# Performance work log

Measured on AMD Instinct MI355X. Metric: run time of the kernel, lower is better.

The kernel has to match this reference:

```python
import jax, jax.numpy as jnp
import numpy as np

DT = 1.0            # neuron_config.base_config.dt (ms)
TAU_MEM = 10.0      # membrane time constant (ms)
SURROGATE_BETA = 1.0  # surrogate sigmoid sharpness for spike nonlinearity

B, P = 256, 4096


def setup_inputs() -> dict:
    key = jax.random.key(0)
    k1, k2, k3, k4 = jax.random.split(key, 4)
    return {
        "external_input": jax.random.normal(k1, (B, P), dtype=jnp.float32),
        "lateral_weights": jax.random.normal(k2, (P, P), dtype=jnp.float32) * 0.1,
        "population_activity": jax.random.uniform(k3, (P,), dtype=jnp.float32),
        "v": jax.random.normal(k4, (B, P), dtype=jnp.float32),
        "threshold": jnp.ones((B, P), dtype=jnp.float32),
    }


def reference(external_input, lateral_weights, population_activity, v, threshold):
    P_ = external_input.shape[1]
    # lateral inhibition: zero self-connections (inhibition_mask = eye == 0)
    masked_w = lateral_weights * (1.0 - jnp.eye(P_, dtype=lateral_weights.dtype))
    lateral = population_activity @ masked_w              # [P]
    total_input = external_input - lateral[None, :]        # [B, P]
    # vectorized adaptive-threshold LIF step across the whole population
    decay = jnp.exp(jnp.asarray(-DT / TAU_MEM, dtype=v.dtype))
    v_new = decay * v + total_input                        # [B, P]
    u = (v_new - threshold) / SURROGATE_BETA
    soft = jax.nn.sigmoid(u)
    hard = (v_new > threshold).astype(v.dtype)
    # straight-through spike: hard forward, sigmoid-surrogate gradient
    spikes = jax.lax.stop_gradient(hard - soft) + soft     # [B, P]
    return spikes
```

## Files before the change

kernel.cpp:

```cpp
#include <hip/hip_runtime.h>


#define PP 4096
#define BB 256

using f4 = __attribute__((ext_vector_type(4))) float;

constexpr int ROWS_PER_CHUNK = 32;
constexpr int NCHUNK = PP / ROWS_PER_CHUNK;
constexpr int COLS_PER_TILE = 512;
constexpr int NTILE = PP / COLS_PER_TILE;

__global__ __launch_bounds__(256)
void lateral_partial(const float* __restrict__ w, const float* __restrict__ pa,
                     double* __restrict__ part) {
    const int tile = blockIdx.x & (NTILE - 1);
    const int rch  = blockIdx.x >> 3;
    const int c    = tile * COLS_PER_TILE + (int)threadIdx.x * 2;
    const int r0   = rch * ROWS_PER_CHUNK;
    double a0 = 0.0, a1 = 0.0;
#pragma unroll
    for (int k = 0; k < ROWS_PER_CHUNK; ++k) {
        const int i = r0 + k;
        const double p = (double)pa[i];
        const float2 wv = *reinterpret_cast<const float2*>(w + (size_t)i * PP + c);
        a0 += p * (double)wv.x;
        a1 += p * (double)wv.y;
    }
    *reinterpret_cast<double2*>(part + (size_t)rch * PP + c) = make_double2(a0, a1);
}

__global__ __launch_bounds__(256)
void lateral_reduce(const double* __restrict__ part, const float* __restrict__ w,
                    const float* __restrict__ pa, double* __restrict__ lat) {
    __shared__ double sh[256];
    const int t   = (int)threadIdx.x;
    const int cj  = t & 31;
    const int grp = t >> 5;
    const int col = blockIdx.x * 32 + cj;
    double s = 0.0;
#pragma unroll
    for (int k = 0; k < NCHUNK / 8; ++k)
        s += part[(size_t)(grp * (NCHUNK / 8) + k) * PP + col];
    sh[t] = s;
    __syncthreads();
    if (t < 128) sh[t] += sh[t + 128];
    __syncthreads();
    if (t < 64)  sh[t] += sh[t + 64];
    __syncthreads();
    if (t < 32) {
        double r = sh[t] + sh[t + 32];
        lat[col] = r - (double)pa[col] * (double)w[(size_t)col * (PP + 1)];
    }
}

__global__ __launch_bounds__(256)
void spike(const float* __restrict__ ext, const float* __restrict__ v,
           const float* __restrict__ thr, const double* __restrict__ lat,
           float* __restrict__ out) {
    const size_t t = ((size_t)blockIdx.x * 256 + threadIdx.x) * 4;
    const int j = (int)(t & (PP - 1));
    const f4 e  = *reinterpret_cast<const f4*>(ext + t);
    const f4 vv = *reinterpret_cast<const f4*>(v + t);
    const f4 th = *reinterpret_cast<const f4*>(thr + t);
    const double2 lA = *reinterpret_cast<const double2*>(lat + j);
    const double2 lB = *reinterpret_cast<const double2*>(lat + j + 2);
    const double dec = 0.90483741803595952;
    f4 o;
    o.x = (dec * (double)vv.x + (double)e.x - lA.x > (double)th.x) ? 1.0f : 0.0f;
    o.y = (dec * (double)vv.y + (double)e.y - lA.y > (double)th.y) ? 1.0f : 0.0f;
    o.z = (dec * (double)vv.z + (double)e.z - lB.x > (double)th.z) ? 1.0f : 0.0f;
    o.w = (dec * (double)vv.w + (double)e.w - lB.y > (double)th.w) ? 1.0f : 0.0f;
    *reinterpret_cast<f4*>(out + t) = o;
}

extern "C" void kernel_launch(void* const* d_in, const int* in_sizes, int n_in,
                              void* d_out, int out_size, void* d_ws, size_t ws_size,
                              hipStream_t stream) {
    const float* ext = (const float*)d_in[0];
    const float* w   = (const float*)d_in[1];
    const float* pa  = (const float*)d_in[2];
    const float* v   = (const float*)d_in[3];
    const float* thr = (const float*)d_in[4];
    float* out = (float*)d_out;

    double* part = (double*)d_ws;
    double* lat  = part + (size_t)NCHUNK * PP;

    lateral_partial<<<NTILE * NCHUNK, 256, 0, stream>>>(w, pa, part);
    lateral_reduce<<<PP / 32, 256, 0, stream>>>(part, w, pa, lat);
    spike<<<(BB * PP) / (4 * 256), 256, 0, stream>>>(ext, v, thr, lat, out);
}
```

Measured before the change: 112.3 us.

## Fuse lateral reduction into spike kernel and stage partials in output buffer

Merges the column reduction and the spike evaluation into one kernel, so each block reduces 16 columns and then writes the spikes for all 256 batch rows of those columns. This drops one launch and the global round trip through the lateral vector. The partial sums now live in the output buffer rather than the workspace. Their layout is interleaved so that each block only overwrites its own partials, and only after it has read them. The partial kernel also now loads four columns per thread. The trade-off is that the spike phase makes narrow 64-byte row accesses that coalesce less well than the earlier fully contiguous pass.

After: 111.9 us. About the same (-0.3%).

```diff
diff --git a/kernel.cpp b/kernel.cpp
--- a/kernel.cpp
+++ b/kernel.cpp
@@ -8,70 +8,84 @@
 
 constexpr int ROWS_PER_CHUNK = 32;
 constexpr int NCHUNK = PP / ROWS_PER_CHUNK;
-constexpr int COLS_PER_TILE = 512;
+constexpr int COLS_PER_TILE = 1024;
 constexpr int NTILE = PP / COLS_PER_TILE;
+constexpr int STRIPE = 16;
+constexpr int NSTRIPE = PP / STRIPE;
 
 __global__ __launch_bounds__(256)
 void lateral_partial(const float* __restrict__ w, const float* __restrict__ pa,
-                     double* __restrict__ part) {
+                     double* __restrict__ pd) {
     const int tile = blockIdx.x & (NTILE - 1);
-    const int rch  = blockIdx.x >> 3;
-    const int c    = tile * COLS_PER_TILE + (int)threadIdx.x * 2;
+    const int rch  = blockIdx.x >> 2;
+    const int c    = tile * COLS_PER_TILE + (int)threadIdx.x * 4;
     const int r0   = rch * ROWS_PER_CHUNK;
-    double a0 = 0.0, a1 = 0.0;
+    double a0 = 0.0, a1 = 0.0, a2 = 0.0, a3 = 0.0;
 #pragma unroll
     for (int k = 0; k < ROWS_PER_CHUNK; ++k) {
         const int i = r0 + k;
         const double p = (double)pa[i];
-        const float2 wv = *reinterpret_cast<const float2*>(w + (size_t)i * PP + c);
+        const f4 wv = *reinterpret_cast<const f4*>(w + (size_t)i * PP + c);
         a0 += p * (double)wv.x;
         a1 += p * (double)wv.y;
+        a2 += p * (double)wv.z;
+        a3 += p * (double)wv.w;
     }
-    *reinterpret_cast<double2*>(part + (size_t)rch * PP + c) = make_double2(a0, a1);
+    const size_t b = (size_t)rch * PP + (c >> 1);
+    *reinterpret_cast<double2*>(pd + b)          = make_double2(a0, a1);
+    *reinterpret_cast<double2*>(pd + b + PP / 2) = make_double2(a2, a3);
 }
 
 __global__ __launch_bounds__(256)
-void lateral_reduce(const double* __restrict__ part, const float* __restrict__ w,
-                    const float* __restrict__ pa, double* __restrict__ lat) {
+void reduce_spike(const double* pd, const float* __restrict__ w,
+                  const float* __restrict__ pa, const float* __restrict__ ext,
+                  const float* __restrict__ v, const float* __restrict__ thr,
+                  float* out) {
     __shared__ double sh[256];
-    const int t   = (int)threadIdx.x;
-    const int cj  = t & 31;
-    const int grp = t >> 5;
-    const int col = blockIdx.x * 32 + cj;
+    __shared__ double lat[STRIPE];
+    const int t  = (int)threadIdx.x;
+    const int c0 = (int)blockIdx.x * STRIPE;
+    const int cj = t & (STRIPE - 1);
+    const int g  = t >> 4;
+    const int c  = c0 + cj;
+    const size_t off = (size_t)(((c & ~3) >> 1) + (c & 1) + ((c >> 1) & 1) * (PP / 2));
     double s = 0.0;
 #pragma unroll
-    for (int k = 0; k < NCHUNK / 8; ++k)
-        s += part[(size_t)(grp * (NCHUNK / 8) + k) * PP + col];
+    for (int k = 0; k < NCHUNK / 16; ++k)
+        s += pd[(size_t)(g * 8 + k) * PP + off];
     sh[t] = s;
     __syncthreads();
     if (t < 128) sh[t] += sh[t + 128];
     __syncthreads();
     if (t < 64)  sh[t] += sh[t + 64];
     __syncthreads();
-    if (t < 32) {
-        double r = sh[t] + sh[t + 32];
-        lat[col] = r - (double)pa[col] * (double)w[(size_t)col * (PP + 1)];
+    if (t < 32)  sh[t] += sh[t + 32];
+    __syncthreads();
+    if (t < 16) {
+        const double r = sh[t] + sh[t + 16];
+        const int cc = c0 + t;
+        lat[t] = r - (double)pa[cc] * (double)w[(size_t)cc * (PP + 1)];
     }
-}
-
-__global__ __launch_bounds__(256)
-void spike(const float* __restrict__ ext, const float* __restrict__ v,
-           const float* __restrict__ thr, const double* __restrict__ lat,
-           float* __restrict__ out) {
-    const size_t t = ((size_t)blockIdx.x * 256 + threadIdx.x) * 4;
-    const int j = (int)(t & (PP - 1));
-    const f4 e  = *reinterpret_cast<const f4*>(ext + t);
-    const f4 vv = *reinterpret_cast<const f4*>(v + t);
-    const f4 th = *reinterpret_cast<const f4*>(thr + t);
-    const double2 lA = *reinterpret_cast<const double2*>(lat + j);
-    const double2 lB = *reinterpret_cast<const double2*>(lat + j + 2);
+    __syncthreads();
+    const int q    = t & 3;
+    const int rowg = t >> 2;
     const double dec = 0.90483741803595952;
-    f4 o;
-    o.x = (dec * (double)vv.x + (double)e.x - lA.x > (double)th.x) ? 1.0f : 0.0f;
-    o.y = (dec * (double)vv.y + (double)e.y - lA.y > (double)th.y) ? 1.0f : 0.0f;
-    o.z = (dec * (double)vv.z + (double)e.z - lB.x > (double)th.z) ? 1.0f : 0.0f;
-    o.w = (dec * (double)vv.w + (double)e.w - lB.y > (double)th.w) ? 1.0f : 0.0f;
-    *reinterpret_cast<f4*>(out + t) = o;
+    const double l0 = lat[q * 4 + 0], l1 = lat[q * 4 + 1];
+    const double l2 = lat[q * 4 + 2], l3 = lat[q * 4 + 3];
+#pragma unroll
+    for (int i = 0; i < 4; ++i) {
+        const int r = rowg * 4 + i;
+        const size_t idx = (size_t)r * PP + c0 + q * 4;
+        const f4 e  = *reinterpret_cast<const f4*>(ext + idx);
+        const f4 vv = *reinterpret_cast<const f4*>(v + idx);
+        const f4 th = *reinterpret_cast<const f4*>(thr + idx);
+        f4 o;
+        o.x = (dec * (double)vv.x + (double)e.x - l0 > (double)th.x) ? 1.0f : 0.0f;
+        o.y = (dec * (double)vv.y + (double)e.y - l1 > (double)th.y) ? 1.0f : 0.0f;
+        o.z = (dec * (double)vv.z + (double)e.z - l2 > (double)th.z) ? 1.0f : 0.0f;
+        o.w = (dec * (double)vv.w + (double)e.w - l3 > (double)th.w) ? 1.0f : 0.0f;
+        *reinterpret_cast<f4*>(out + idx) = o;
+    }
 }
 
 extern "C" void kernel_launch(void* const* d_in, const int* in_sizes, int n_in,
@@ -83,11 +97,8 @@
     const float* v   = (const float*)d_in[3];
     const float* thr = (const float*)d_in[4];
     float* out = (float*)d_out;
+    double* pd = (double*)d_out;
 
-    double* part = (double*)d_ws;
-    double* lat  = part + (size_t)NCHUNK * PP;
-
-    lateral_partial<<<NTILE * NCHUNK, 256, 0, stream>>>(w, pa, part);
-    lateral_reduce<<<PP / 32, 256, 0, stream>>>(part, w, pa, lat);
-    spike<<<(BB * PP) / (4 * 256), 256, 0, stream>>>(ext, v, thr, lat, out);
+    lateral_partial<<<NTILE * NCHUNK, 256, 0, stream>>>(w, pa, pd);
+    reduce_spike<<<NSTRIPE, 256, 0, stream>>>(pd, w, pa, ext, v, thr, out);
 }
```
